# Performance work log

Hardware: AMD Instinct MI355X
Metric: run time of the kernel (lower is better)

The kernel has to match this reference:

```python
import jax, jax.numpy as jnp
import numpy as np

N_NODES = 50000
N_EDGES = 800000
IN_CH, HID, OUT_CH = 128, 256, 40


def setup_inputs() -> dict:
    key = jax.random.key(0)
    ks = jax.random.split(key, 10)
    x = jax.random.normal(ks[0], (N_NODES, IN_CH), dtype=jnp.float32)
    edge_index = jax.random.randint(ks[1], (2, N_EDGES), 0, N_NODES, dtype=jnp.int64)
    s = 0.05  # weight init scale
    return {
        "x": x,
        "edge_index": edge_index,
        "W1a": jax.random.normal(ks[2], (IN_CH, HID), dtype=jnp.float32) * s,
        "b1a": jnp.zeros((HID,), jnp.float32),
        "W2a": jax.random.normal(ks[3], (HID, HID), dtype=jnp.float32) * s,
        "b2a": jnp.zeros((HID,), jnp.float32),
        "W1b": jax.random.normal(ks[4], (HID, HID), dtype=jnp.float32) * s,
        "b1b": jnp.zeros((HID,), jnp.float32),
        "W2b": jax.random.normal(ks[5], (HID, HID), dtype=jnp.float32) * s,
        "b2b": jnp.zeros((HID,), jnp.float32),
        "Wlin": jax.random.normal(ks[6], (HID * 2, OUT_CH), dtype=jnp.float32) * s,
        "blin": jnp.zeros((OUT_CH,), jnp.float32),
    }


def _gin_conv(h, src, dst, W1, b1, W2, b2):
    # sum-aggregate messages h[src] into destination nodes, eps = 0
    agg = jax.ops.segment_sum(h[src], dst, num_segments=N_NODES)
    z = h + agg
    z = jnp.maximum(z @ W1 + b1, 0.0) @ W2 + b2  # 2-layer MLP
    return z


def reference(x, edge_index, W1a, b1a, W2a, b2a, W1b, b1b, W2b, b2b, Wlin, blin):
    src, dst = edge_index[0], edge_index[1]
    h1 = jnp.maximum(_gin_conv(x, src, dst, W1a, b1a, W2a, b2a), 0.0)
    h2 = jnp.maximum(_gin_conv(h1, src, dst, W1b, b1b, W2b, b2b), 0.0)
    h_cat = jnp.concatenate([h1, h2], axis=1)  # [N, 2*HID]
    logits = h_cat @ Wlin + blin
    return jax.nn.log_softmax(logits, axis=1)
```

## Files before the change

kernel.cpp:

```cpp
#include <hip/hip_runtime.h>
#include <math.h>

#define N_NODES 50000
#define N_EDGES 800000
#define IN_CH 128
#define HID 256
#define OUT_CH 40
#define GRP 6250
#define NCHUNK 32
#define TS 264

typedef unsigned short u16;
typedef unsigned char u8;
typedef __attribute__((ext_vector_type(8))) short bf16x8;
typedef __attribute__((ext_vector_type(8))) unsigned short u16x8;
typedef __attribute__((ext_vector_type(4))) float f32x4;
typedef __attribute__((ext_vector_type(2))) float f32x2;

__device__ __forceinline__ float bf2f(u16 u) {
    union { unsigned int i; float f; } v; v.i = ((unsigned int)u) << 16; return v.f;
}
__device__ __forceinline__ u16 f2bf(float f) {
    union { float f; unsigned int i; } v; v.f = f;
    unsigned int x = v.i;
    x += 0x7fffu + ((x >> 16) & 1u);
    return (u16)(x >> 16);
}

#define GLOBAL_AS __attribute__((address_space(1)))
#define LDS_AS __attribute__((address_space(3)))
__device__ __forceinline__ void async_cp16(const void* g, void* l) {
    __builtin_amdgcn_global_load_lds((const GLOBAL_AS unsigned int*)g,
                                     (LDS_AS unsigned int*)l, 16, 0, 0);
}

__device__ __forceinline__ void pack_w(
    const float* __restrict__ in, u16* __restrict__ out, int K, int N, int c)
{
    for (int k = threadIdx.x; k < K; k += 256) {
        int kk32 = k >> 5, quad = (k >> 3) & 3, e = k & 7;
        size_t base = (((size_t)c * (K >> 5) + kk32) * 64 + quad * 16) * 8 + e;
#pragma unroll
        for (int li = 0; li < 16; li++) {
            int n = c * 16 + li;
            float v = (n < N) ? in[(size_t)k * N + n] : 0.f;
            out[base + (size_t)li * 8] = f2bf(v);
        }
    }
}

__global__ __launch_bounds__(256) void prep_fused(
    const float* __restrict__ x, u16* __restrict__ xb, u8* __restrict__ xf8,
    const int* __restrict__ ei, u16* __restrict__ e16,
    const float* __restrict__ W1a, const float* __restrict__ W2a,
    const float* __restrict__ W1b, const float* __restrict__ W2b,
    const float* __restrict__ Wlin,
    u16* __restrict__ W1aPk, u16* __restrict__ W2aPk,
    u16* __restrict__ W1bPk, u16* __restrict__ W2bPk, u16* __restrict__ WlinPk)
{
    int b = blockIdx.x;
    if (b < 6250) {
        int i = b * 256 + threadIdx.x;
        float4 v = ((const float4*)x)[i];
        ushort4 o;
        o.x = f2bf(v.x); o.y = f2bf(v.y); o.z = f2bf(v.z); o.w = f2bf(v.w);
        ((ushort4*)xb)[i] = o;
        int p = __builtin_amdgcn_cvt_pk_fp8_f32(v.x, v.y, 0, false);
        p = __builtin_amdgcn_cvt_pk_fp8_f32(v.z, v.w, p, true);
        ((unsigned int*)xf8)[i] = (unsigned int)p;
    } else if (b < 7813) {
        int i = (b - 6250) * 256 + threadIdx.x;
        if (i < (2 * N_EDGES) / 4) {
            int4 v = ((const int4*)ei)[i];
            ushort4 o;
            o.x = (u16)v.x; o.y = (u16)v.y; o.z = (u16)v.z; o.w = (u16)v.w;
            ((ushort4*)e16)[i] = o;
        }
    } else {
        int t = b - 7813;
        if (t < 16)       pack_w(W1a, W1aPk, IN_CH, HID, t);
        else if (t < 32)  pack_w(W2a, W2aPk, HID, HID, t - 16);
        else if (t < 48)  pack_w(W1b, W1bPk, HID, HID, t - 32);
        else if (t < 64)  pack_w(W2b, W2bPk, HID, HID, t - 48);
        else              pack_w(Wlin, WlinPk, 2 * HID, OUT_CH, t - 64);
    }
}

__global__ __launch_bounds__(256) void hist_priv(
    const u16* __restrict__ dst16, u16* __restrict__ partial)
{
    __shared__ int hist[GRP];
    const int b = blockIdx.x;
    const int g = b & 7;
    const int sub = b >> 3;
    const int lo = g * GRP;
    const int CH = N_EDGES / NCHUNK;
    for (int i = threadIdx.x; i < GRP; i += 256) hist[i] = 0;
    __syncthreads();
    const ushort4* dsts = (const ushort4*)(dst16 + sub * CH);
    for (int k = threadIdx.x; k < CH / 4; k += 256) {
        ushort4 d = dsts[k];
        int r0 = (int)d.x - lo, r1 = (int)d.y - lo;
        int r2 = (int)d.z - lo, r3 = (int)d.w - lo;
        if ((unsigned)r0 < (unsigned)GRP) atomicAdd(&hist[r0], 1);
        if ((unsigned)r1 < (unsigned)GRP) atomicAdd(&hist[r1], 1);
        if ((unsigned)r2 < (unsigned)GRP) atomicAdd(&hist[r2], 1);
        if ((unsigned)r3 < (unsigned)GRP) atomicAdd(&hist[r3], 1);
    }
    __syncthreads();
    u16* po = partial + (size_t)b * GRP;
    for (int i = threadIdx.x; i < GRP; i += 256) po[i] = (u16)hist[i];
}

__global__ __launch_bounds__(256) void deg_cp(
    const u16* __restrict__ partial, u16* __restrict__ chunkpref,
    u16* __restrict__ deg16)
{
    int node = blockIdx.x * 256 + threadIdx.x;
    if (node >= N_NODES) return;
    int g = node / GRP;
    int off = node - g * GRP;
    int d = 0;
#pragma unroll
    for (int sub = 0; sub < NCHUNK; sub++) {
        chunkpref[(size_t)sub * N_NODES + node] = (u16)d;
        d += partial[(size_t)(sub * 8 + g) * GRP + off];
    }
    deg16[node] = (u16)d;
}

__global__ __launch_bounds__(256) void scan1(
    const u16* __restrict__ deg16, int* __restrict__ excl,
    int* __restrict__ partials_out)
{
    __shared__ int lds[256];
    const int tid = threadIdx.x;
    const int base = blockIdx.x * 1024 + tid * 4;
    int v[4]; int s = 0;
#pragma unroll
    for (int i = 0; i < 4; i++) {
        int idx = base + i;
        int d = (idx < N_NODES) ? (int)deg16[idx] : 0;
        v[i] = d;
        s += d;
    }
    lds[tid] = s;
    __syncthreads();
    for (int off = 1; off < 256; off <<= 1) {
        int t = (tid >= off) ? lds[tid - off] : 0;
        __syncthreads();
        lds[tid] += t;
        __syncthreads();
    }
    int run = lds[tid] - s;
#pragma unroll
    for (int i = 0; i < 4; i++) {
        int idx = base + i;
        if (idx < N_NODES) excl[idx] = run;
        run += v[i];
    }
    if (tid == 255) partials_out[blockIdx.x] = lds[255];
}

__global__ __launch_bounds__(256) void scan3(
    int* __restrict__ excl, const int* __restrict__ partials,
    int* __restrict__ sentinel, int nPart)
{
    __shared__ int bp[64];
    const int tid = threadIdx.x;
    if (tid < 64) {
        int orig = (tid < nPart) ? partials[tid] : 0;
        int v = orig;
#pragma unroll
        for (int off = 1; off < 64; off <<= 1) {
            int t = __shfl_up(v, off, 64);
            if (tid >= off) v += t;
        }
        bp[tid] = v - orig;
    }
    __syncthreads();
    int idx = blockIdx.x * 256 + tid;
    if (idx < N_NODES) {
        int r = excl[idx] + bp[idx >> 10];
        excl[idx] = r;
    }
    if (idx == 0) sentinel[0] = N_EDGES;
}

__global__ __launch_bounds__(256) void csr_fill(
    const u16* __restrict__ src16, const u16* __restrict__ dst16,
    const int* __restrict__ rowp, const u16* __restrict__ chunkpref,
    u16* __restrict__ csr_src)
{
    __shared__ int cur[GRP];
    const int g = blockIdx.x & 7;
    const int c = blockIdx.x >> 3;
    const int lo = g * GRP;
    const int CH = N_EDGES / NCHUNK;
    const u16* cp = chunkpref + (size_t)c * N_NODES + lo;
    for (int i = threadIdx.x; i < GRP; i += 256)
        cur[i] = rowp[lo + i] + cp[i];
    __syncthreads();
    const ushort4* dsts = (const ushort4*)(dst16 + c * CH);
    const ushort4* srcs = (const ushort4*)(src16 + c * CH);
    for (int k = threadIdx.x; k < CH / 4; k += 256) {
        ushort4 d = dsts[k];
        ushort4 sc = srcs[k];
        int r0 = (int)d.x - lo, r1 = (int)d.y - lo;
        int r2 = (int)d.z - lo, r3 = (int)d.w - lo;
        if ((unsigned)r0 < (unsigned)GRP) { int p = atomicAdd(&cur[r0], 1); csr_src[p] = sc.x; }
        if ((unsigned)r1 < (unsigned)GRP) { int p = atomicAdd(&cur[r1], 1); csr_src[p] = sc.y; }
        if ((unsigned)r2 < (unsigned)GRP) { int p = atomicAdd(&cur[r2], 1); csr_src[p] = sc.z; }
        if ((unsigned)r3 < (unsigned)GRP) { int p = atomicAdd(&cur[r3], 1); csr_src[p] = sc.w; }
    }
}


__global__ __launch_bounds__(256) void gather_agg_f8_128(
    const u16* __restrict__ feat_bf, const u8* __restrict__ feat_f8,
    const int* __restrict__ row_ptr, const int* __restrict__ row_end,
    const u16* __restrict__ csr_src, u16* __restrict__ out)
{
    const int tid = threadIdx.x;
    const int lane = tid & 63;
    const int wv = tid >> 6;
    const int li = lane & 7;
    int node = blockIdx.x * 32 + wv * 8 + (lane >> 3);
    const bool valid = node < N_NODES;
    if (!valid) node = N_NODES - 1;

    int j = row_ptr[node];
    int deg = valid ? (row_end[node] - j) : 0;

    float acc[16];
    {
        u16x8 s0 = *(const u16x8*)(feat_bf + (size_t)node * IN_CH + li * 16);
        u16x8 s1 = *(const u16x8*)(feat_bf + (size_t)node * IN_CH + li * 16 + 8);
#pragma unroll
        for (int q = 0; q < 8; q++) { acc[q] = bf2f(s0[q]); acc[8 + q] = bf2f(s1[q]); }
    }

    int maxdeg = deg;
#pragma unroll
    for (int off = 8; off < 64; off <<= 1)
        maxdeg = max(maxdeg, __shfl_xor(maxdeg, off, 64));

    for (int it = 0; it < maxdeg; it += 4) {
        int4 g0 = {0,0,0,0}, g1 = {0,0,0,0}, g2 = {0,0,0,0}, g3 = {0,0,0,0};
        if (it < deg)
            g0 = *(const int4*)(feat_f8 + (size_t)csr_src[j + it] * IN_CH + li * 16);
        if (it + 1 < deg)
            g1 = *(const int4*)(feat_f8 + (size_t)csr_src[j + it + 1] * IN_CH + li * 16);
        if (it + 2 < deg)
            g2 = *(const int4*)(feat_f8 + (size_t)csr_src[j + it + 2] * IN_CH + li * 16);
        if (it + 3 < deg)
            g3 = *(const int4*)(feat_f8 + (size_t)csr_src[j + it + 3] * IN_CH + li * 16);
#pragma unroll
        for (int q = 0; q < 4; q++) {
            int w0 = (&g0.x)[q], w1 = (&g1.x)[q], w2 = (&g2.x)[q], w3 = (&g3.x)[q];
            f32x2 l0 = __builtin_amdgcn_cvt_pk_f32_fp8(w0, false);
            f32x2 h0 = __builtin_amdgcn_cvt_pk_f32_fp8(w0, true);
            f32x2 l1 = __builtin_amdgcn_cvt_pk_f32_fp8(w1, false);
            f32x2 h1 = __builtin_amdgcn_cvt_pk_f32_fp8(w1, true);
            f32x2 l2 = __builtin_amdgcn_cvt_pk_f32_fp8(w2, false);
            f32x2 h2 = __builtin_amdgcn_cvt_pk_f32_fp8(w2, true);
            f32x2 l3 = __builtin_amdgcn_cvt_pk_f32_fp8(w3, false);
            f32x2 h3 = __builtin_amdgcn_cvt_pk_f32_fp8(w3, true);
            acc[q * 4 + 0] += (l0.x + l1.x) + (l2.x + l3.x);
            acc[q * 4 + 1] += (l0.y + l1.y) + (l2.y + l3.y);
            acc[q * 4 + 2] += (h0.x + h1.x) + (h2.x + h3.x);
            acc[q * 4 + 3] += (h0.y + h1.y) + (h2.y + h3.y);
        }
    }

    if (valid) {
        u16x8 o0, o1;
#pragma unroll
        for (int q = 0; q < 8; q++) { o0[q] = f2bf(acc[q]); o1[q] = f2bf(acc[8 + q]); }
        *(u16x8*)(out + (size_t)node * IN_CH + li * 16) = o0;
        *(u16x8*)(out + (size_t)node * IN_CH + li * 16 + 8) = o1;
    }
}

__global__ __launch_bounds__(256) void gather_agg_f8_256(
    const u16* __restrict__ feat_bf, const u8* __restrict__ feat_f8,
    const int* __restrict__ row_ptr, const int* __restrict__ row_end,
    const u16* __restrict__ csr_src, u16* __restrict__ out)
{
    const int tid = threadIdx.x;
    const int lane = tid & 63;
    const int wv = tid >> 6;
    const int li = lane & 15;
    const int node = blockIdx.x * 16 + wv * 4 + (lane >> 4);

    int j = row_ptr[node];
    int deg = row_end[node] - j;

    float acc[16];
    {
        u16x8 s0 = *(const u16x8*)(feat_bf + (size_t)node * HID + li * 16);
        u16x8 s1 = *(const u16x8*)(feat_bf + (size_t)node * HID + li * 16 + 8);
#pragma unroll
        for (int q = 0; q < 8; q++) { acc[q] = bf2f(s0[q]); acc[8 + q] = bf2f(s1[q]); }
    }

    int maxdeg = deg;
#pragma unroll
    for (int off = 16; off < 64; off <<= 1)
        maxdeg = max(maxdeg, __shfl_xor(maxdeg, off, 64));

    for (int it = 0; it < maxdeg; it += 4) {
        int4 g0 = {0,0,0,0}, g1 = {0,0,0,0}, g2 = {0,0,0,0}, g3 = {0,0,0,0};
        if (it < deg)
            g0 = *(const int4*)(feat_f8 + (size_t)csr_src[j + it] * HID + li * 16);
        if (it + 1 < deg)
            g1 = *(const int4*)(feat_f8 + (size_t)csr_src[j + it + 1] * HID + li * 16);
        if (it + 2 < deg)
            g2 = *(const int4*)(feat_f8 + (size_t)csr_src[j + it + 2] * HID + li * 16);
        if (it + 3 < deg)
            g3 = *(const int4*)(feat_f8 + (size_t)csr_src[j + it + 3] * HID + li * 16);
#pragma unroll
        for (int q = 0; q < 4; q++) {
            int w0 = (&g0.x)[q], w1 = (&g1.x)[q], w2 = (&g2.x)[q], w3 = (&g3.x)[q];
            f32x2 l0 = __builtin_amdgcn_cvt_pk_f32_fp8(w0, false);
            f32x2 h0 = __builtin_amdgcn_cvt_pk_f32_fp8(w0, true);
            f32x2 l1 = __builtin_amdgcn_cvt_pk_f32_fp8(w1, false);
            f32x2 h1 = __builtin_amdgcn_cvt_pk_f32_fp8(w1, true);
            f32x2 l2 = __builtin_amdgcn_cvt_pk_f32_fp8(w2, false);
            f32x2 h2 = __builtin_amdgcn_cvt_pk_f32_fp8(w2, true);
            f32x2 l3 = __builtin_amdgcn_cvt_pk_f32_fp8(w3, false);
            f32x2 h3 = __builtin_amdgcn_cvt_pk_f32_fp8(w3, true);
            acc[q * 4 + 0] += (l0.x + l1.x) + (l2.x + l3.x);
            acc[q * 4 + 1] += (l0.y + l1.y) + (l2.y + l3.y);
            acc[q * 4 + 2] += (h0.x + h1.x) + (h2.x + h3.x);
            acc[q * 4 + 3] += (h0.y + h1.y) + (h2.y + h3.y);
        }
    }

    u16x8 o0, o1;
#pragma unroll
    for (int q = 0; q < 8; q++) { o0[q] = f2bf(acc[q]); o1[q] = f2bf(acc[8 + q]); }
    *(u16x8*)(out + (size_t)node * HID + li * 16) = o0;
    *(u16x8*)(out + (size_t)node * HID + li * 16 + 8) = o1;
}

__global__ __launch_bounds__(256, 4) void mlp_fused(
    const u16* __restrict__ A, int K1,
    const u16* __restrict__ W1pk, const float* __restrict__ b1,
    const u16* __restrict__ W2pk, const float* __restrict__ b2,
    u16* __restrict__ out, u8* __restrict__ outF8, int M)
{
    __shared__ u16 SB[64 * TS];

    const int tid = threadIdx.x;
    const int lane = tid & 63;
    const int wid = tid >> 6;
    const int li = lane & 15;
    const int quad = lane >> 4;
    const int koff = quad * 8;
    const int row0 = blockIdx.x * 64;
    const int KB1 = K1 >> 5;
    const int rsh = (K1 == 256) ? 9 : 8;

    {
        const u8* Ag = (const u8*)(A + (size_t)row0 * K1);
        const int rounds = K1 >> 5;
        for (int j = 0; j < rounds; j++) {
            int L = (j * 256 + tid) * 16;
            int G = L ^ (((L >> rsh) & 7) << 4);
            async_cp16(Ag + G, (u8*)SB + L);
        }
    }

    f32x4 acc[4][4];
#pragma unroll
    for (int i = 0; i < 4; i++)
#pragma unroll
        for (int j = 0; j < 4; j++) acc[i][j] = (f32x4){0.f, 0.f, 0.f, 0.f};

#define LDW(WF, WPK, KB, KK32)                                                \
    {   _Pragma("unroll")                                                     \
        for (int t = 0; t < 4; t++)                                           \
            WF[t] = *(const bf16x8*)((WPK) +                                  \
                (((size_t)(wid * 4 + t) * (KB) + (KK32)) * 64 + lane) * 8); }
#define LDA1(AF, KK)                                                          \
    {   _Pragma("unroll")                                                     \
        for (int t = 0; t < 4; t++) {                                         \
            int row = t * 16 + li;                                            \
            int bo = row * (K1 * 2) + ((KK) + koff) * 2;                      \
            bo ^= (row & 7) << 4;                                             \
            AF[t] = *(const bf16x8*)((const u8*)SB + bo); } }
#define LDA2(AF, KK)                                                          \
    {   _Pragma("unroll")                                                     \
        for (int t = 0; t < 4; t++)                                           \
            AF[t] = *(const bf16x8*)(SB + (t * 16 + li) * TS + (KK) + koff); }
#define MFMA16(AF, WF)                                                        \
    {   _Pragma("unroll")                                                     \
        for (int mt = 0; mt < 4; mt++)                                        \
            _Pragma("unroll")                                                 \
            for (int nt = 0; nt < 4; nt++)                                    \
                acc[mt][nt] = __builtin_amdgcn_mfma_f32_16x16x32_bf16(        \
                    AF[mt], WF[nt], acc[mt][nt], 0, 0, 0); }

    bf16x8 wfA[4], wfB[4], af[4];

    LDW(wfA, W1pk, KB1, 0);
    __syncthreads();

    for (int kk32 = 0; kk32 < KB1; kk32 += 2) {
        LDW(wfB, W1pk, KB1, kk32 + 1);
        LDA1(af, kk32 * 32);
        MFMA16(af, wfA);
        if (kk32 + 2 < KB1) LDW(wfA, W1pk, KB1, kk32 + 2);
        LDA1(af, kk32 * 32 + 32);
        MFMA16(af, wfB);
    }
    __syncthreads();

#pragma unroll
    for (int nt = 0; nt < 4; nt++) {
        int col = wid * 64 + nt * 16 + li;
        float bv = b1[col];
#pragma unroll
        for (int mt = 0; mt < 4; mt++) {
#pragma unroll
            for (int reg = 0; reg < 4; reg++) {
                int row = mt * 16 + quad * 4 + reg;
                float v = fmaxf(acc[mt][nt][reg] + bv, 0.f);
                SB[row * TS + col] = f2bf(v);
                acc[mt][nt][reg] = 0.f;
            }
        }
    }
    LDW(wfA, W2pk, 8, 0);
    __syncthreads();

    for (int kk32 = 0; kk32 < 8; kk32 += 2) {
        LDW(wfB, W2pk, 8, kk32 + 1);
        LDA2(af, kk32 * 32);
        MFMA16(af, wfA);
        if (kk32 + 2 < 8) LDW(wfA, W2pk, 8, kk32 + 2);
        LDA2(af, kk32 * 32 + 32);
        MFMA16(af, wfB);
    }
#undef LDW
#undef LDA1
#undef LDA2
#undef MFMA16

    __syncthreads();
#pragma unroll
    for (int nt = 0; nt < 4; nt++) {
        int col = wid * 64 + nt * 16 + li;
        float bv = b2[col];
#pragma unroll
        for (int mt = 0; mt < 4; mt++) {
#pragma unroll
            for (int reg = 0; reg < 4; reg++) {
                int row = mt * 16 + quad * 4 + reg;
                float v = fmaxf(acc[mt][nt][reg] + bv, 0.f);
                SB[row * TS + col] = f2bf(v);
            }
        }
    }
    __syncthreads();
#pragma unroll
    for (int it = 0; it < 8; it++) {
        int flat = it * 4096 + tid * 16;
        int r = flat >> 9;
        int cu = (flat & 511) >> 1;
        int row = row0 + r;
        if (row < M) {
            u16x8 v = *(const u16x8*)(SB + r * TS + cu);
            *(u16x8*)(out + (size_t)row * HID + cu) = v;
            if (outF8 != nullptr) {
                int p0 = __builtin_amdgcn_cvt_pk_fp8_f32(bf2f(v[0]), bf2f(v[1]), 0, false);
                p0 = __builtin_amdgcn_cvt_pk_fp8_f32(bf2f(v[2]), bf2f(v[3]), p0, true);
                int p1 = __builtin_amdgcn_cvt_pk_fp8_f32(bf2f(v[4]), bf2f(v[5]), 0, false);
                p1 = __builtin_amdgcn_cvt_pk_fp8_f32(bf2f(v[6]), bf2f(v[7]), p1, true);
                int2 pv; pv.x = p0; pv.y = p1;
                *(int2*)(outF8 + (size_t)row * HID + cu) = pv;
            }
        }
    }
}

__global__ __launch_bounds__(256, 6) void gemm_mfma(
    const u16* __restrict__ A, const u16* __restrict__ Acat, int Ksplit, int ldA,
    const u16* __restrict__ Bpk, const float* __restrict__ bias,
    float* __restrict__ out, int M, int K)
{
    const int tid = threadIdx.x;
    const int lane = tid & 63;
    const int wid = tid >> 6;
    const int li = lane & 15;
    const int quad = lane >> 4;
    const int koff = quad * 8;
    const int row0 = blockIdx.x * 64 + wid * 16;

    f32x4 acc[3];
#pragma unroll
    for (int i = 0; i < 3; i++) acc[i] = (f32x4){0.f, 0.f, 0.f, 0.f};

    int r = row0 + li;
    const int arow = (r < M) ? r : (M - 1);
    const int KB = K >> 5;

#define LD_G(AF, BF, KK)                                                      \
    {   const u16* Ab = ((KK) >= Ksplit) ? Acat : A;                          \
        const int kb = ((KK) >= Ksplit) ? ((KK) - Ksplit) : (KK);             \
        AF = *(const bf16x8*)(Ab + (size_t)arow * ldA + kb + koff);           \
        _Pragma("unroll")                                                     \
        for (int t = 0; t < 3; t++)                                           \
            BF[t] = *(const bf16x8*)(Bpk +                                    \
                (((size_t)t * KB + ((KK) >> 5)) * 64 + lane) * 8); }
#define MFMA3(AF, BF)                                                         \
    {   _Pragma("unroll")                                                     \
        for (int nt = 0; nt < 3; nt++)                                        \
            acc[nt] = __builtin_amdgcn_mfma_f32_16x16x32_bf16(                \
                AF, BF[nt], acc[nt], 0, 0, 0); }

    {
        bf16x8 a0, b0[3], a1, b1v[3];
        LD_G(a0, b0, 0);
        for (int kk = 0; kk < K; kk += 64) {
            LD_G(a1, b1v, kk + 32);
            MFMA3(a0, b0);
            if (kk + 64 < K) LD_G(a0, b0, kk + 64);
            MFMA3(a1, b1v);
        }
    }
#undef LD_G
#undef MFMA3

    float b0v = bias[li];
    float b1s = bias[16 + li];
    float b2s = (li < 8) ? bias[32 + li] : 0.f;
#pragma unroll
    for (int reg = 0; reg < 4; reg++) {
        int row = row0 + quad * 4 + reg;
        float v0 = acc[0][reg] + b0v;
        float v1 = acc[1][reg] + b1s;
        float v2 = (li < 8) ? (acc[2][reg] + b2s) : -INFINITY;
        float m = fmaxf(fmaxf(v0, v1), v2);
#pragma unroll
        for (int off = 1; off < 16; off <<= 1)
            m = fmaxf(m, __shfl_xor(m, off, 64));
        float s = expf(v0 - m) + expf(v1 - m)
                + ((li < 8) ? expf(v2 - m) : 0.f);
#pragma unroll
        for (int off = 1; off < 16; off <<= 1)
            s += __shfl_xor(s, off, 64);
        float lg = m + logf(s);
        if (row < M) {
            out[(size_t)row * OUT_CH + li] = v0 - lg;
            out[(size_t)row * OUT_CH + 16 + li] = v1 - lg;
            if (li < 8) out[(size_t)row * OUT_CH + 32 + li] = v2 - lg;
        }
    }
}

extern "C" void kernel_launch(void* const* d_in, const int* in_sizes, int n_in,
                              void* d_out, int out_size, void* d_ws, size_t ws_size,
                              hipStream_t stream)
{
    const float* x    = (const float*)d_in[0];
    const int*   ei   = (const int*)d_in[1];
    const float* W1a  = (const float*)d_in[2];
    const float* b1a  = (const float*)d_in[3];
    const float* W2a  = (const float*)d_in[4];
    const float* b2a  = (const float*)d_in[5];
    const float* W1b  = (const float*)d_in[6];
    const float* b1b  = (const float*)d_in[7];
    const float* W2b  = (const float*)d_in[8];
    const float* b2b  = (const float*)d_in[9];
    const float* Wlin = (const float*)d_in[10];
    const float* blin = (const float*)d_in[11];
    float* out = (float*)d_out;

    const size_t R = (size_t)N_NODES * HID;
    u16* R0 = (u16*)d_ws;
    u16* R1 = R0 + R;
    u16* R2 = R1 + R;
    u16* R3 = R2 + R;
    u16* R4 = R3 + R;
    u16* xbf = R0;
    u16* zA  = R1;
    u16* partial = (u16*)R1;
    u8*  xf8 = (u8*)(R1 + (size_t)N_NODES * IN_CH);
    u8*  h1f8 = (u8*)R1;
    u16* h1  = R3;
    u16* zB  = R4;
    u16* h2  = R2;

    u16* wts = R4 + R;
    u16* W1aPk = wts;
    u16* W2aPk = W1aPk + 256 * 128;
    u16* W1bPk = W2aPk + 256 * 256;
    u16* W2bPk = W1bPk + 256 * 256;
    u16* WlinPk = W2bPk + 256 * 256;
    int* rowp   = (int*)(WlinPk + 128 * 512);
    int* cursor = rowp + N_NODES;
    int* part   = cursor + N_NODES;
    u16* csr    = (u16*)(part + 64);
    u16* e16    = csr + N_EDGES;
    u16* src16  = e16;
    u16* dst16  = e16 + N_EDGES;
    u16* chunkpref = dst16 + N_EDGES;
    u16* deg16  = chunkpref + (size_t)NCHUNK * N_NODES;

    dim3 blk(256);
    const int scanBlocks = (N_NODES + 1023) / 1024;
    const int degBlocks  = (N_NODES + 255) / 256;
    const int agg128Blocks = (N_NODES + 31) / 32;
    const int agg256Blocks = N_NODES / 16;
    const int mlpBlocks  = (N_NODES + 63) / 64;
    const int gemmBlocks = (N_NODES + 63) / 64;

    prep_fused<<<7880, blk, 0, stream>>>(x, xbf, xf8, ei, e16,
                                         W1a, W2a, W1b, W2b, Wlin,
                                         W1aPk, W2aPk, W1bPk, W2bPk, WlinPk);
    hist_priv<<<8 * NCHUNK, blk, 0, stream>>>(dst16, partial);
    deg_cp<<<degBlocks, blk, 0, stream>>>(partial, chunkpref, deg16);
    scan1<<<scanBlocks, blk, 0, stream>>>(deg16, rowp, part);
    scan3<<<(N_NODES + 255) / 256, blk, 0, stream>>>(rowp, part, cursor, scanBlocks);
    csr_fill<<<8 * NCHUNK, blk, 0, stream>>>(src16, dst16, rowp, chunkpref, csr);

    gather_agg_f8_128<<<agg128Blocks, blk, 0, stream>>>(xbf, xf8, rowp, rowp + 1, csr, zA);
    mlp_fused<<<mlpBlocks, blk, 0, stream>>>(zA, IN_CH, W1aPk, b1a, W2aPk, b2a,
                                             h1, h1f8, N_NODES);

    gather_agg_f8_256<<<agg256Blocks, blk, 0, stream>>>(h1, h1f8, rowp, rowp + 1, csr, zB);
    mlp_fused<<<mlpBlocks, blk, 0, stream>>>(zB, HID, W1bPk, b1b, W2bPk, b2b,
                                             h2, nullptr, N_NODES);

    gemm_mfma<<<gemmBlocks, blk, 0, stream>>>(h1, h2, HID, HID, WlinPk, blin,
                                              out, N_NODES, 2 * HID);
}
```

Measured before the change: 257.8 us.

## Fuse neighbor gather-aggregation into the GIN MLP kernels and halve histogram LDS groups

Folds the sparse gather-sum directly into the fused MLP kernel. Each block aggregates its 64 nodes straight into shared memory and feeds that tile to the MFMA GEMMs, so the separate aggregation kernels and their global z round-trip go away. Degrees now come from deg16 instead of row_end differences. Separately, the histogram and CSR-fill kernels split each node group in half, which doubles block count and halves LDS per block for more occupancy. The trade-off is that the latency-bound gather now runs inside an MFMA kernel limited to 4 blocks per CU, which may reduce the parallelism available to hide gather latency.

```diff
diff --git a/kernel.cpp b/kernel.cpp
--- a/kernel.cpp
+++ b/kernel.cpp
@@ -7,6 +7,7 @@
 #define HID 256
 #define OUT_CH 40
 #define GRP 6250
+#define HGRP 3125
 #define NCHUNK 32
 #define TS 264
 
@@ -25,13 +26,6 @@
     unsigned int x = v.i;
     x += 0x7fffu + ((x >> 16) & 1u);
     return (u16)(x >> 16);
-}
-
-#define GLOBAL_AS __attribute__((address_space(1)))
-#define LDS_AS __attribute__((address_space(3)))
-__device__ __forceinline__ void async_cp16(const void* g, void* l) {
-    __builtin_amdgcn_global_load_lds((const GLOBAL_AS unsigned int*)g,
-                                     (LDS_AS unsigned int*)l, 16, 0, 0);
 }
 
 __device__ __forceinline__ void pack_w(
@@ -89,27 +83,27 @@
 __global__ __launch_bounds__(256) void hist_priv(
     const u16* __restrict__ dst16, u16* __restrict__ partial)
 {
-    __shared__ int hist[GRP];
+    __shared__ int hist[HGRP];
     const int b = blockIdx.x;
-    const int g = b & 7;
-    const int sub = b >> 3;
-    const int lo = g * GRP;
+    const int gh = b & 15;
+    const int sub = b >> 4;
+    const int lo = gh * HGRP;
     const int CH = N_EDGES / NCHUNK;
-    for (int i = threadIdx.x; i < GRP; i += 256) hist[i] = 0;
+    for (int i = threadIdx.x; i < HGRP; i += 256) hist[i] = 0;
     __syncthreads();
     const ushort4* dsts = (const ushort4*)(dst16 + sub * CH);
     for (int k = threadIdx.x; k < CH / 4; k += 256) {
         ushort4 d = dsts[k];
         int r0 = (int)d.x - lo, r1 = (int)d.y - lo;
         int r2 = (int)d.z - lo, r3 = (int)d.w - lo;
-        if ((unsigned)r0 < (unsigned)GRP) atomicAdd(&hist[r0], 1);
-        if ((unsigned)r1 < (unsigned)GRP) atomicAdd(&hist[r1], 1);
-        if ((unsigned)r2 < (unsigned)GRP) atomicAdd(&hist[r2], 1);
-        if ((unsigned)r3 < (unsigned)GRP) atomicAdd(&hist[r3], 1);
-    }
-    __syncthreads();
-    u16* po = partial + (size_t)b * GRP;
-    for (int i = threadIdx.x; i < GRP; i += 256) po[i] = (u16)hist[i];
+        if ((unsigned)r0 < (unsigned)HGRP) atomicAdd(&hist[r0], 1);
+        if ((unsigned)r1 < (unsigned)HGRP) atomicAdd(&hist[r1], 1);
+        if ((unsigned)r2 < (unsigned)HGRP) atomicAdd(&hist[r2], 1);
+        if ((unsigned)r3 < (unsigned)HGRP) atomicAdd(&hist[r3], 1);
+    }
+    __syncthreads();
+    u16* po = partial + (size_t)(sub * 8 + (gh >> 1)) * GRP + (gh & 1) * HGRP;
+    for (int i = threadIdx.x; i < HGRP; i += 256) po[i] = (u16)hist[i];
 }
 
 __global__ __launch_bounds__(256) void deg_cp(
@@ -192,13 +186,13 @@
     const int* __restrict__ rowp, const u16* __restrict__ chunkpref,
     u16* __restrict__ csr_src)
 {
-    __shared__ int cur[GRP];
-    const int g = blockIdx.x & 7;
-    const int c = blockIdx.x >> 3;
-    const int lo = g * GRP;
+    __shared__ int cur[HGRP];
+    const int gh = blockIdx.x & 15;
+    const int c = blockIdx.x >> 4;
+    const int lo = gh * HGRP;
     const int CH = N_EDGES / NCHUNK;
     const u16* cp = chunkpref + (size_t)c * N_NODES + lo;
-    for (int i = threadIdx.x; i < GRP; i += 256)
+    for (int i = threadIdx.x; i < HGRP; i += 256)
         cur[i] = rowp[lo + i] + cp[i];
     __syncthreads();
     const ushort4* dsts = (const ushort4*)(dst16 + c * CH);
@@ -208,144 +202,17 @@
         ushort4 sc = srcs[k];
         int r0 = (int)d.x - lo, r1 = (int)d.y - lo;
         int r2 = (int)d.z - lo, r3 = (int)d.w - lo;
-        if ((unsigned)r0 < (unsigned)GRP) { int p = atomicAdd(&cur[r0], 1); csr_src[p] = sc.x; }
-        if ((unsigned)r1 < (unsigned)GRP) { int p = atomicAdd(&cur[r1], 1); csr_src[p] = sc.y; }
-        if ((unsigned)r2 < (unsigned)GRP) { int p = atomicAdd(&cur[r2], 1); csr_src[p] = sc.z; }
-        if ((unsigned)r3 < (unsigned)GRP) { int p = atomicAdd(&cur[r3], 1); csr_src[p] = sc.w; }
-    }
-}
-
-
-__global__ __launch_bounds__(256) void gather_agg_f8_128(
-    const u16* __restrict__ feat_bf, const u8* __restrict__ feat_f8,
-    const int* __restrict__ row_ptr, const int* __restrict__ row_end,
-    const u16* __restrict__ csr_src, u16* __restrict__ out)
-{
-    const int tid = threadIdx.x;
-    const int lane = tid & 63;
-    const int wv = tid >> 6;
-    const int li = lane & 7;
-    int node = blockIdx.x * 32 + wv * 8 + (lane >> 3);
-    const bool valid = node < N_NODES;
-    if (!valid) node = N_NODES - 1;
-
-    int j = row_ptr[node];
-    int deg = valid ? (row_end[node] - j) : 0;
-
-    float acc[16];
-    {
-        u16x8 s0 = *(const u16x8*)(feat_bf + (size_t)node * IN_CH + li * 16);
-        u16x8 s1 = *(const u16x8*)(feat_bf + (size_t)node * IN_CH + li * 16 + 8);
-#pragma unroll
-        for (int q = 0; q < 8; q++) { acc[q] = bf2f(s0[q]); acc[8 + q] = bf2f(s1[q]); }
-    }
-
-    int maxdeg = deg;
-#pragma unroll
-    for (int off = 8; off < 64; off <<= 1)
-        maxdeg = max(maxdeg, __shfl_xor(maxdeg, off, 64));
-
-    for (int it = 0; it < maxdeg; it += 4) {
-        int4 g0 = {0,0,0,0}, g1 = {0,0,0,0}, g2 = {0,0,0,0}, g3 = {0,0,0,0};
-        if (it < deg)
-            g0 = *(const int4*)(feat_f8 + (size_t)csr_src[j + it] * IN_CH + li * 16);
-        if (it + 1 < deg)
-            g1 = *(const int4*)(feat_f8 + (size_t)csr_src[j + it + 1] * IN_CH + li * 16);
-        if (it + 2 < deg)
-            g2 = *(const int4*)(feat_f8 + (size_t)csr_src[j + it + 2] * IN_CH + li * 16);
-        if (it + 3 < deg)
-            g3 = *(const int4*)(feat_f8 + (size_t)csr_src[j + it + 3] * IN_CH + li * 16);
-#pragma unroll
-        for (int q = 0; q < 4; q++) {
-            int w0 = (&g0.x)[q], w1 = (&g1.x)[q], w2 = (&g2.x)[q], w3 = (&g3.x)[q];
-            f32x2 l0 = __builtin_amdgcn_cvt_pk_f32_fp8(w0, false);
-            f32x2 h0 = __builtin_amdgcn_cvt_pk_f32_fp8(w0, true);
-            f32x2 l1 = __builtin_amdgcn_cvt_pk_f32_fp8(w1, false);
-            f32x2 h1 = __builtin_amdgcn_cvt_pk_f32_fp8(w1, true);
-            f32x2 l2 = __builtin_amdgcn_cvt_pk_f32_fp8(w2, false);
-            f32x2 h2 = __builtin_amdgcn_cvt_pk_f32_fp8(w2, true);
-            f32x2 l3 = __builtin_amdgcn_cvt_pk_f32_fp8(w3, false);
-            f32x2 h3 = __builtin_amdgcn_cvt_pk_f32_fp8(w3, true);
-            acc[q * 4 + 0] += (l0.x + l1.x) + (l2.x + l3.x);
-            acc[q * 4 + 1] += (l0.y + l1.y) + (l2.y + l3.y);
-            acc[q * 4 + 2] += (h0.x + h1.x) + (h2.x + h3.x);
-            acc[q * 4 + 3] += (h0.y + h1.y) + (h2.y + h3.y);
-        }
-    }
-
-    if (valid) {
-        u16x8 o0, o1;
-#pragma unroll
-        for (int q = 0; q < 8; q++) { o0[q] = f2bf(acc[q]); o1[q] = f2bf(acc[8 + q]); }
-        *(u16x8*)(out + (size_t)node * IN_CH + li * 16) = o0;
-        *(u16x8*)(out + (size_t)node * IN_CH + li * 16 + 8) = o1;
-    }
-}
-
-__global__ __launch_bounds__(256) void gather_agg_f8_256(
-    const u16* __restrict__ feat_bf, const u8* __restrict__ feat_f8,
-    const int* __restrict__ row_ptr, const int* __restrict__ row_end,
-    const u16* __restrict__ csr_src, u16* __restrict__ out)
-{
-    const int tid = threadIdx.x;
-    const int lane = tid & 63;
-    const int wv = tid >> 6;
-    const int li = lane & 15;
-    const int node = blockIdx.x * 16 + wv * 4 + (lane >> 4);
-
-    int j = row_ptr[node];
-    int deg = row_end[node] - j;
-
-    float acc[16];
-    {
-        u16x8 s0 = *(const u16x8*)(feat_bf + (size_t)node * HID + li * 16);
-        u16x8 s1 = *(const u16x8*)(feat_bf + (size_t)node * HID + li * 16 + 8);
-#pragma unroll
-        for (int q = 0; q < 8; q++) { acc[q] = bf2f(s0[q]); acc[8 + q] = bf2f(s1[q]); }
-    }
-
-    int maxdeg = deg;
-#pragma unroll
-    for (int off = 16; off < 64; off <<= 1)
-        maxdeg = max(maxdeg, __shfl_xor(maxdeg, off, 64));
-
-    for (int it = 0; it < maxdeg; it += 4) {
-        int4 g0 = {0,0,0,0}, g1 = {0,0,0,0}, g2 = {0,0,0,0}, g3 = {0,0,0,0};
-        if (it < deg)
-            g0 = *(const int4*)(feat_f8 + (size_t)csr_src[j + it] * HID + li * 16);
-        if (it + 1 < deg)
-            g1 = *(const int4*)(feat_f8 + (size_t)csr_src[j + it + 1] * HID + li * 16);
-        if (it + 2 < deg)
-            g2 = *(const int4*)(feat_f8 + (size_t)csr_src[j + it + 2] * HID + li * 16);
-        if (it + 3 < deg)
-            g3 = *(const int4*)(feat_f8 + (size_t)csr_src[j + it + 3] * HID + li * 16);
-#pragma unroll
-        for (int q = 0; q < 4; q++) {
-            int w0 = (&g0.x)[q], w1 = (&g1.x)[q], w2 = (&g2.x)[q], w3 = (&g3.x)[q];
-            f32x2 l0 = __builtin_amdgcn_cvt_pk_f32_fp8(w0, false);
-            f32x2 h0 = __builtin_amdgcn_cvt_pk_f32_fp8(w0, true);
-            f32x2 l1 = __builtin_amdgcn_cvt_pk_f32_fp8(w1, false);
-            f32x2 h1 = __builtin_amdgcn_cvt_pk_f32_fp8(w1, true);
-            f32x2 l2 = __builtin_amdgcn_cvt_pk_f32_fp8(w2, false);
-            f32x2 h2 = __builtin_amdgcn_cvt_pk_f32_fp8(w2, true);
-            f32x2 l3 = __builtin_amdgcn_cvt_pk_f32_fp8(w3, false);
-            f32x2 h3 = __builtin_amdgcn_cvt_pk_f32_fp8(w3, true);
-            acc[q * 4 + 0] += (l0.x + l1.x) + (l2.x + l3.x);
-            acc[q * 4 + 1] += (l0.y + l1.y) + (l2.y + l3.y);
-            acc[q * 4 + 2] += (h0.x + h1.x) + (h2.x + h3.x);
-            acc[q * 4 + 3] += (h0.y + h1.y) + (h2.y + h3.y);
-        }
-    }
-
-    u16x8 o0, o1;
-#pragma unroll
-    for (int q = 0; q < 8; q++) { o0[q] = f2bf(acc[q]); o1[q] = f2bf(acc[8 + q]); }
-    *(u16x8*)(out + (size_t)node * HID + li * 16) = o0;
-    *(u16x8*)(out + (size_t)node * HID + li * 16 + 8) = o1;
-}
-
-__global__ __launch_bounds__(256, 4) void mlp_fused(
-    const u16* __restrict__ A, int K1,
+        if ((unsigned)r0 < (unsigned)HGRP) { int p = atomicAdd(&cur[r0], 1); csr_src[p] = sc.x; }
+        if ((unsigned)r1 < (unsigned)HGRP) { int p = atomicAdd(&cur[r1], 1); csr_src[p] = sc.y; }
+        if ((unsigned)r2 < (unsigned)HGRP) { int p = atomicAdd(&cur[r2], 1); csr_src[p] = sc.z; }
+        if ((unsigned)r3 < (unsigned)HGRP) { int p = atomicAdd(&cur[r3], 1); csr_src[p] = sc.w; }
+    }
+}
+
+__global__ __launch_bounds__(256, 4) void gmlp_fused(
+    const u16* __restrict__ feat_bf, const u8* __restrict__ feat_f8, int K1,
+    const int* __restrict__ rowp, const u16* __restrict__ deg16,
+    const u16* __restrict__ csr_src,
     const u16* __restrict__ W1pk, const float* __restrict__ b1,
     const u16* __restrict__ W2pk, const float* __restrict__ b2,
     u16* __restrict__ out, u8* __restrict__ outF8, int M)
@@ -360,37 +227,13 @@
     const int koff = quad * 8;
     const int row0 = blockIdx.x * 64;
     const int KB1 = K1 >> 5;
-    const int rsh = (K1 == 256) ? 9 : 8;
-
-    {
-        const u8* Ag = (const u8*)(A + (size_t)row0 * K1);
-        const int rounds = K1 >> 5;
-        for (int j = 0; j < rounds; j++) {
-            int L = (j * 256 + tid) * 16;
-            int G = L ^ (((L >> rsh) & 7) << 4);
-            async_cp16(Ag + G, (u8*)SB + L);
-        }
-    }
-
-    f32x4 acc[4][4];
-#pragma unroll
-    for (int i = 0; i < 4; i++)
-#pragma unroll
-        for (int j = 0; j < 4; j++) acc[i][j] = (f32x4){0.f, 0.f, 0.f, 0.f};
 
 #define LDW(WF, WPK, KB, KK32)                                                \
     {   _Pragma("unroll")                                                     \
         for (int t = 0; t < 4; t++)                                           \
             WF[t] = *(const bf16x8*)((WPK) +                                  \
                 (((size_t)(wid * 4 + t) * (KB) + (KK32)) * 64 + lane) * 8); }
-#define LDA1(AF, KK)                                                          \
-    {   _Pragma("unroll")                                                     \
-        for (int t = 0; t < 4; t++) {                                         \
-            int row = t * 16 + li;                                            \
-            int bo = row * (K1 * 2) + ((KK) + koff) * 2;                      \
-            bo ^= (row & 7) << 4;                                             \
-            AF[t] = *(const bf16x8*)((const u8*)SB + bo); } }
-#define LDA2(AF, KK)                                                          \
+#define LDA(AF, KK)                                                           \
     {   _Pragma("unroll")                                                     \
         for (int t = 0; t < 4; t++)                                           \
             AF[t] = *(const bf16x8*)(SB + (t * 16 + li) * TS + (KK) + koff); }
@@ -403,16 +246,129 @@
                     AF[mt], WF[nt], acc[mt][nt], 0, 0, 0); }
 
     bf16x8 wfA[4], wfB[4], af[4];
-
     LDW(wfA, W1pk, KB1, 0);
+
+    if (K1 == 256) {
+#pragma unroll
+        for (int iter = 0; iter < 4; iter++) {
+            int nl = iter * 16 + wid * 4 + (lane >> 4);
+            int node = row0 + nl;
+            if (node >= M) node = M - 1;
+            int j = rowp[node];
+            int deg = deg16[node];
+            float acc1[16];
+            {
+                u16x8 s0 = *(const u16x8*)(feat_bf + (size_t)node * 256 + li * 16);
+                u16x8 s1 = *(const u16x8*)(feat_bf + (size_t)node * 256 + li * 16 + 8);
+#pragma unroll
+                for (int q = 0; q < 8; q++) { acc1[q] = bf2f(s0[q]); acc1[8 + q] = bf2f(s1[q]); }
+            }
+            int maxdeg = deg;
+#pragma unroll
+            for (int off = 16; off < 64; off <<= 1)
+                maxdeg = max(maxdeg, __shfl_xor(maxdeg, off, 64));
+            for (int it = 0; it < maxdeg; it += 4) {
+                int4 g0 = {0,0,0,0}, g1 = {0,0,0,0}, g2 = {0,0,0,0}, g3 = {0,0,0,0};
+                if (it < deg)
+                    g0 = *(const int4*)(feat_f8 + (size_t)csr_src[j + it] * 256 + li * 16);
+                if (it + 1 < deg)
+                    g1 = *(const int4*)(feat_f8 + (size_t)csr_src[j + it + 1] * 256 + li * 16);
+                if (it + 2 < deg)
+                    g2 = *(const int4*)(feat_f8 + (size_t)csr_src[j + it + 2] * 256 + li * 16);
+                if (it + 3 < deg)
+                    g3 = *(const int4*)(feat_f8 + (size_t)csr_src[j + it + 3] * 256 + li * 16);
+#pragma unroll
+                for (int q = 0; q < 4; q++) {
+                    int w0 = (&g0.x)[q], w1 = (&g1.x)[q], w2 = (&g2.x)[q], w3 = (&g3.x)[q];
+                    f32x2 l0 = __builtin_amdgcn_cvt_pk_f32_fp8(w0, false);
+                    f32x2 h0 = __builtin_amdgcn_cvt_pk_f32_fp8(w0, true);
+                    f32x2 l1 = __builtin_amdgcn_cvt_pk_f32_fp8(w1, false);
+                    f32x2 h1 = __builtin_amdgcn_cvt_pk_f32_fp8(w1, true);
+                    f32x2 l2 = __builtin_amdgcn_cvt_pk_f32_fp8(w2, false);
+                    f32x2 h2 = __builtin_amdgcn_cvt_pk_f32_fp8(w2, true);
+                    f32x2 l3 = __builtin_amdgcn_cvt_pk_f32_fp8(w3, false);
+                    f32x2 h3 = __builtin_amdgcn_cvt_pk_f32_fp8(w3, true);
+                    acc1[q * 4 + 0] += (l0.x + l1.x) + (l2.x + l3.x);
+                    acc1[q * 4 + 1] += (l0.y + l1.y) + (l2.y + l3.y);
+                    acc1[q * 4 + 2] += (h0.x + h1.x) + (h2.x + h3.x);
+                    acc1[q * 4 + 3] += (h0.y + h1.y) + (h2.y + h3.y);
+                }
+            }
+            u16x8 o0, o1;
+#pragma unroll
+            for (int q = 0; q < 8; q++) { o0[q] = f2bf(acc1[q]); o1[q] = f2bf(acc1[8 + q]); }
+            *(u16x8*)(SB + nl * TS + li * 16) = o0;
+            *(u16x8*)(SB + nl * TS + li * 16 + 8) = o1;
+        }
+    } else {
+        const int li8 = lane & 7;
+#pragma unroll
+        for (int iter = 0; iter < 2; iter++) {
+            int nl = iter * 32 + wid * 8 + (lane >> 3);
+            int node = row0 + nl;
+            if (node >= M) node = M - 1;
+            int j = rowp[node];
+            int deg = deg16[node];
+            float acc1[16];
+            {
+                u16x8 s0 = *(const u16x8*)(feat_bf + (size_t)node * 128 + li8 * 16);
+                u16x8 s1 = *(const u16x8*)(feat_bf + (size_t)node * 128 + li8 * 16 + 8);
+#pragma unroll
+                for (int q = 0; q < 8; q++) { acc1[q] = bf2f(s0[q]); acc1[8 + q] = bf2f(s1[q]); }
+            }
+            int maxdeg = deg;
+#pragma unroll
+            for (int off = 8; off < 64; off <<= 1)
+                maxdeg = max(maxdeg, __shfl_xor(maxdeg, off, 64));
+            for (int it = 0; it < maxdeg; it += 4) {
+                int4 g0 = {0,0,0,0}, g1 = {0,0,0,0}, g2 = {0,0,0,0}, g3 = {0,0,0,0};
+                if (it < deg)
+                    g0 = *(const int4*)(feat_f8 + (size_t)csr_src[j + it] * 128 + li8 * 16);
+                if (it + 1 < deg)
+                    g1 = *(const int4*)(feat_f8 + (size_t)csr_src[j + it + 1] * 128 + li8 * 16);
+                if (it + 2 < deg)
+                    g2 = *(const int4*)(feat_f8 + (size_t)csr_src[j + it + 2] * 128 + li8 * 16);
+                if (it + 3 < deg)
+                    g3 = *(const int4*)(feat_f8 + (size_t)csr_src[j + it + 3] * 128 + li8 * 16);
+#pragma unroll
+                for (int q = 0; q < 4; q++) {
+                    int w0 = (&g0.x)[q], w1 = (&g1.x)[q], w2 = (&g2.x)[q], w3 = (&g3.x)[q];
+                    f32x2 l0 = __builtin_amdgcn_cvt_pk_f32_fp8(w0, false);
+                    f32x2 h0 = __builtin_amdgcn_cvt_pk_f32_fp8(w0, true);
+                    f32x2 l1 = __builtin_amdgcn_cvt_pk_f32_fp8(w1, false);
+                    f32x2 h1 = __builtin_amdgcn_cvt_pk_f32_fp8(w1, true);
+                    f32x2 l2 = __builtin_amdgcn_cvt_pk_f32_fp8(w2, false);
+                    f32x2 h2 = __builtin_amdgcn_cvt_pk_f32_fp8(w2, true);
+                    f32x2 l3 = __builtin_amdgcn_cvt_pk_f32_fp8(w3, false);
+                    f32x2 h3 = __builtin_amdgcn_cvt_pk_f32_fp8(w3, true);
+                    acc1[q * 4 + 0] += (l0.x + l1.x) + (l2.x + l3.x);
+                    acc1[q * 4 + 1] += (l0.y + l1.y) + (l2.y + l3.y);
+                    acc1[q * 4 + 2] += (h0.x + h1.x) + (h2.x + h3.x);
+                    acc1[q * 4 + 3] += (h0.y + h1.y) + (h2.y + h3.y);
+                }
+            }
+            u16x8 o0, o1;
+#pragma unroll
+            for (int q = 0; q < 8; q++) { o0[q] = f2bf(acc1[q]); o1[q] = f2bf(acc1[8 + q]); }
+            *(u16x8*)(SB + nl * TS + li8 * 16) = o0;
+            *(u16x8*)(SB + nl * TS + li8 * 16 + 8) = o1;
+        }
+    }
+
+    f32x4 acc[4][4];
+#pragma unroll
+    for (int i = 0; i < 4; i++)
+#pragma unroll
+        for (int j = 0; j < 4; j++) acc[i][j] = (f32x4){0.f, 0.f, 0.f, 0.f};
+
     __syncthreads();
 
     for (int kk32 = 0; kk32 < KB1; kk32 += 2) {
         LDW(wfB, W1pk, KB1, kk32 + 1);
-        LDA1(af, kk32 * 32);
+        LDA(af, kk32 * 32);
         MFMA16(af, wfA);
         if (kk32 + 2 < KB1) LDW(wfA, W1pk, KB1, kk32 + 2);
-        LDA1(af, kk32 * 32 + 32);
+        LDA(af, kk32 * 32 + 32);
         MFMA16(af, wfB);
     }
     __syncthreads();
@@ -437,15 +393,14 @@
 
     for (int kk32 = 0; kk32 < 8; kk32 += 2) {
         LDW(wfB, W2pk, 8, kk32 + 1);
-        LDA2(af, kk32 * 32);
+        LDA(af, kk32 * 32);
         MFMA16(af, wfA);
         if (kk32 + 2 < 8) LDW(wfA, W2pk, 8, kk32 + 2);
-        LDA2(af, kk32 * 32 + 32);
+        LDA(af, kk32 * 32 + 32);
         MFMA16(af, wfB);
     }
 #undef LDW
-#undef LDA1
-#undef LDA2
+#undef LDA
 #undef MFMA16
 
     __syncthreads();
@@ -583,25 +538,21 @@
     u16* R1 = R0 + R;
     u16* R2 = R1 + R;
     u16* R3 = R2 + R;
-    u16* R4 = R3 + R;
     u16* xbf = R0;
-    u16* zA  = R1;
     u16* partial = (u16*)R1;
     u8*  xf8 = (u8*)(R1 + (size_t)N_NODES * IN_CH);
     u8*  h1f8 = (u8*)R1;
     u16* h1  = R3;
-    u16* zB  = R4;
     u16* h2  = R2;
 
-    u16* wts = R4 + R;
+    u16* wts = R3 + R;
     u16* W1aPk = wts;
     u16* W2aPk = W1aPk + 256 * 128;
     u16* W1bPk = W2aPk + 256 * 256;
     u16* W2bPk = W1bPk + 256 * 256;
     u16* WlinPk = W2bPk + 256 * 256;
     int* rowp   = (int*)(WlinPk + 128 * 512);
-    int* cursor = rowp + N_NODES;
-    int* part   = cursor + N_NODES;
+    int* part   = rowp + N_NODES + 64;
     u16* csr    = (u16*)(part + 64);
     u16* e16    = csr + N_EDGES;
     u16* src16  = e16;
@@ -612,27 +563,25 @@
     dim3 blk(256);
     const int scanBlocks = (N_NODES + 1023) / 1024;
     const int degBlocks  = (N_NODES + 255) / 256;
-    const int agg128Blocks = (N_NODES + 31) / 32;
-    const int agg256Blocks = N_NODES / 16;
     const int mlpBlocks  = (N_NODES + 63) / 64;
     const int gemmBlocks = (N_NODES + 63) / 64;
 
     prep_fused<<<7880, blk, 0, stream>>>(x, xbf, xf8, ei, e16,
                                          W1a, W2a, W1b, W2b, Wlin,
                                          W1aPk, W2aPk, W1bPk, W2bPk, WlinPk);
-    hist_priv<<<8 * NCHUNK, blk, 0, stream>>>(dst16, partial);
+    hist_priv<<<16 * NCHUNK, blk, 0, stream>>>(dst16, partial);
     deg_cp<<<degBlocks, blk, 0, stream>>>(partial, chunkpref, deg16);
     scan1<<<scanBlocks, blk, 0, stream>>>(deg16, rowp, part);
-    scan3<<<(N_NODES + 255) / 256, blk, 0, stream>>>(rowp, part, cursor, scanBlocks);
-    csr_fill<<<8 * NCHUNK, blk, 0, stream>>>(src16, dst16, rowp, chunkpref, csr);
-
-    gather_agg_f8_128<<<agg128Blocks, blk, 0, stream>>>(xbf, xf8, rowp, rowp + 1, csr, zA);
-    mlp_fused<<<mlpBlocks, blk, 0, stream>>>(zA, IN_CH, W1aPk, b1a, W2aPk, b2a,
-                                             h1, h1f8, N_NODES);
-
-    gather_agg_f8_256<<<agg256Blocks, blk, 0, stream>>>(h1, h1f8, rowp, rowp + 1, csr, zB);
-    mlp_fused<<<mlpBlocks, blk, 0, stream>>>(zB, HID, W1bPk, b1b, W2bPk, b2b,
-                                             h2, nullptr, N_NODES);
+    scan3<<<(N_NODES + 255) / 256, blk, 0, stream>>>(rowp, part, rowp + N_NODES, scanBlocks);
+    csr_fill<<<16 * NCHUNK, blk, 0, stream>>>(src16, dst16, rowp, chunkpref, csr);
+
+    gmlp_fused<<<mlpBlocks, blk, 0, stream>>>(xbf, xf8, IN_CH, rowp, deg16, csr,
+                                              W1aPk, b1a, W2aPk, b2a,
+                                              h1, h1f8, N_NODES);
+
+    gmlp_fused<<<mlpBlocks, blk, 0, stream>>>(h1, h1f8, HID, rowp, deg16, csr,
+                                              W1bPk, b1b, W2bPk, b2b,
+                                              h2, nullptr, N_NODES);
 
     gemm_mfma<<<gemmBlocks, blk, 0, stream>>>(h1, h2, HID, HID, WlinPk, blin,
                                               out, N_NODES, 2 * HID);
```

New measurement: 270.1 us. +4.8%, slower.
